# Kernel tuning notes

Hardware: AMD Instinct MI355X
Metric: run time of the kernel (lower is better)

## Reference

```python
import jax, jax.numpy as jnp
import numpy as np

HIDDEN = 2048
N_EXPERTS = 8
TOP_K = 2
MOE_INTER = 1408
NORM_TOPK = False  # config.norm_topk_prob


def setup_inputs() -> dict:
    key = jax.random.key(0)
    k0, k1, k2, k3, k4 = jax.random.split(key, 5)
    hidden_states = jax.random.normal(k0, (2, 2048, HIDDEN), dtype=jnp.float32)
    # router gate: nn.Linear(hidden, num_experts, bias=False) -> store as [H, E]
    gate_w = jax.random.normal(k1, (HIDDEN, N_EXPERTS), dtype=jnp.float32) * 0.02
    # per-expert MLP weights, stacked over experts (Linear is x @ W.T, stored pre-transposed)
    w_gate = jax.random.normal(k2, (N_EXPERTS, HIDDEN, MOE_INTER), dtype=jnp.float32) * 0.02
    w_up = jax.random.normal(k3, (N_EXPERTS, HIDDEN, MOE_INTER), dtype=jnp.float32) * 0.02
    w_down = jax.random.normal(k4, (N_EXPERTS, MOE_INTER, HIDDEN), dtype=jnp.float32) * 0.02
    return {"hidden_states": hidden_states, "gate_w": gate_w,
            "w_gate": w_gate, "w_up": w_up, "w_down": w_down}


def reference(hidden_states, gate_w, w_gate, w_up, w_down):
    B, S, H = hidden_states.shape
    x = hidden_states.reshape(-1, H)                      # [T, H]
    T = x.shape[0]
    router_logits = x @ gate_w                            # [T, E]
    probs = jax.nn.softmax(router_logits.astype(jnp.float32), axis=-1)
    routing_weights, selected = jax.lax.top_k(probs, TOP_K)  # [T, K], [T, K]
    if NORM_TOPK:
        routing_weights = routing_weights / routing_weights.sum(-1, keepdims=True)
    routing_weights = routing_weights.astype(x.dtype)
    # dense combine weights [T, E]: scatter top-k weights to expert slots
    combine = jnp.zeros((T, N_EXPERTS), dtype=x.dtype)
    combine = combine.at[jnp.arange(T)[:, None], selected].add(routing_weights)
    # run all experts densely (reference form of gather-MLP-scatter)
    g = jnp.einsum('th,ehf->tef', x, w_gate)              # [T, E, F]
    u = jnp.einsum('th,ehf->tef', x, w_up)
    h = jax.nn.silu(g) * u
    y = jnp.einsum('tef,efh->teh', h, w_down)             # [T, E, H]
    out = jnp.einsum('te,teh->th', combine, y)            # [T, H]
    return out
```

## Files before the change

kernel.cpp:

```cpp
#include <hip/hip_runtime.h>
#include <hip/hip_bf16.h>

#define HID  2048
#define NEXP 8
#define FINT 1408
#define TM   128
#define BK   32
#define GU_NPAN 88
#define DN_NPAN 64

typedef __bf16 bf16_t;
typedef __bf16 bf16x8 __attribute__((ext_vector_type(8)));
typedef float  f32x4  __attribute__((ext_vector_type(4)));

#define AS1 __attribute__((address_space(1)))
#define AS3 __attribute__((address_space(3)))

__device__ __forceinline__ void gll16(const void* g, void* l) {
    __builtin_amdgcn_global_load_lds((const AS1 void*)g, (AS3 void*)l, 16, 0, 0);
}

#define VMCNT6() asm volatile("s_waitcnt vmcnt(6)" ::: "memory")
#define VMCNT0() asm volatile("s_waitcnt vmcnt(0)" ::: "memory")
#define SB0() __builtin_amdgcn_sched_barrier(0)

__global__ __launch_bounds__(64) void router_kernel(
    const float* __restrict__ x, const float* __restrict__ gw,
    int* __restrict__ cnt, int* __restrict__ topk_id, float* __restrict__ topk_w,
    bf16_t* __restrict__ xb, int T)
{
    int t = blockIdx.x;
    if (t >= T) return;
    int lane = threadIdx.x;
    float acc[NEXP];
#pragma unroll
    for (int e = 0; e < NEXP; ++e) acc[e] = 0.f;
    const float* xr = x + (size_t)t * HID;
    bf16_t* xo = xb + (size_t)t * HID;
    for (int i0 = lane * 4; i0 < HID; i0 += 256) {
        float4 xv = *(const float4*)(xr + i0);
        bf16_t b4[4] = {(bf16_t)xv.x, (bf16_t)xv.y, (bf16_t)xv.z, (bf16_t)xv.w};
        *(uint2*)(xo + i0) = *(uint2*)b4;
        float xs[4] = {xv.x, xv.y, xv.z, xv.w};
#pragma unroll
        for (int u = 0; u < 4; ++u) {
            const float4* g4 = (const float4*)(gw + (size_t)(i0 + u) * NEXP);
            float4 a = g4[0], b = g4[1];
            acc[0] += xs[u] * a.x; acc[1] += xs[u] * a.y; acc[2] += xs[u] * a.z; acc[3] += xs[u] * a.w;
            acc[4] += xs[u] * b.x; acc[5] += xs[u] * b.y; acc[6] += xs[u] * b.z; acc[7] += xs[u] * b.w;
        }
    }
#pragma unroll
    for (int d = 1; d < 64; d <<= 1) {
#pragma unroll
        for (int e = 0; e < NEXP; ++e) acc[e] += __shfl_xor(acc[e], d, 64);
    }
    float mx = acc[0];
#pragma unroll
    for (int e = 1; e < NEXP; ++e) mx = fmaxf(mx, acc[e]);
    float p[NEXP]; float s = 0.f;
#pragma unroll
    for (int e = 0; e < NEXP; ++e) { p[e] = expf(acc[e] - mx); s += p[e]; }
    float inv = 1.f / s;
    int i1 = 0;
#pragma unroll
    for (int e = 1; e < NEXP; ++e) if (acc[e] > acc[i1]) i1 = e;
    int i2 = (i1 == 0) ? 1 : 0;
#pragma unroll
    for (int e = 0; e < NEXP; ++e) if (e != i1 && acc[e] > acc[i2]) i2 = e;
    if (lane == 0) {
        topk_id[t * 2 + 0] = i1; topk_id[t * 2 + 1] = i2;
        topk_w[t * 2 + 0] = p[i1] * inv; topk_w[t * 2 + 1] = p[i2] * inv;
        atomicAdd(&cnt[i1], 1); atomicAdd(&cnt[i2], 1);
    }
}

__global__ void offsets_kernel(const int* __restrict__ cnt, int* __restrict__ offs,
                               int* __restrict__ gbase, int* __restrict__ gcount,
                               int* __restrict__ dbase, int* __restrict__ dcount,
                               int* __restrict__ gu, int* __restrict__ dn)
{
    __shared__ int gc[8], dc[8];
    int tid = threadIdx.x;
    if (tid == 0) {
        int s = 0;
        for (int e = 0; e < NEXP; ++e) { offs[e] = s; s += cnt[e]; }
        offs[NEXP] = s;
    }
    if (tid < 8) {
        int c = 0;
        for (int p = tid; p < GU_NPAN; p += 8) { int e = p / 11; c += (cnt[e] + TM - 1) / TM; }
        gc[tid] = c;
    } else if (tid < 16) {
        int x = tid - 8, c = 0;
        for (int p = x; p < DN_NPAN; p += 8) { int e = p >> 3; c += (cnt[e] + TM - 1) / TM; }
        dc[x] = c;
    }
    __syncthreads();
    if (tid < 8) {
        int base = 0;
        for (int i = 0; i < tid; ++i) base += gc[i];
        gbase[tid] = base; gcount[tid] = gc[tid];
        int k = base;
        for (int p = tid; p < GU_NPAN; p += 8) {
            int e = p / 11, fp = p - e * 11;
            int nt = (cnt[e] + TM - 1) / TM;
            for (int t = 0; t < nt; ++t) gu[k++] = (e << 10) | (fp << 6) | t;
        }
    } else if (tid < 16) {
        int x = tid - 8;
        int base = 0;
        for (int i = 0; i < x; ++i) base += dc[i];
        dbase[x] = base; dcount[x] = dc[x];
        int k = base;
        for (int p = x; p < DN_NPAN; p += 8) {
            int e = p >> 3, hp = p & 7;
            int nt = (cnt[e] + TM - 1) / TM;
            for (int t = 0; t < nt; ++t) dn[k++] = (e << 10) | (hp << 6) | t;
        }
    }
}

__global__ void scatter_kernel(
    const int* __restrict__ topk_id, const int* __restrict__ offs, int* __restrict__ fill,
    int* __restrict__ tok, int* __restrict__ slot_of, int T)
{
    int t = blockIdx.x * blockDim.x + threadIdx.x;
    if (t >= T) return;
#pragma unroll
    for (int k = 0; k < 2; ++k) {
        int e = topk_id[t * 2 + k];
        int pos = atomicAdd(&fill[e], 1);
        int slot = offs[e] + pos;
        tok[slot] = t;
        slot_of[t * 2 + k] = slot;
    }
}

__global__ __launch_bounds__(256) void cvt3_kernel(
    const float* __restrict__ wg, const float* __restrict__ wu, const float* __restrict__ wd,
    bf16_t* __restrict__ wgb, bf16_t* __restrict__ wub, bf16_t* __restrict__ wdb)
{
    const int per = NEXP * (HID / 64) * (FINT / 64);
    int b = blockIdx.x;
    const float* in; bf16_t* outb; int R, C;
    if (b < per)            { in = wg; outb = wgb; R = HID;  C = FINT; }
    else if (b < 2 * per)   { b -= per; in = wu; outb = wub; R = HID;  C = FINT; }
    else                    { b -= 2 * per; in = wd; outb = wdb; R = FINT; C = HID; }

    int tilesC = C >> 6;
    int perE = (R >> 6) * tilesC;
    int e = b / perE;
    int rem = b - e * perE;
    int tr = rem / tilesC, tc = rem - tr * tilesC;
    const float* src = in + (size_t)e * R * C + (size_t)(tr * 64) * C + tc * 64;
    bf16_t* dst = outb + (size_t)e * R * C + (size_t)(tc * 64) * R + tr * 64;

    __shared__ float tile[64][65];
    int tid = threadIdx.x;
    int rr = tid >> 4;
    int cc = (tid & 15) * 4;
#pragma unroll
    for (int i = 0; i < 4; ++i) {
        float4 v = *(const float4*)(src + (size_t)(rr + i * 16) * C + cc);
        tile[rr + i * 16][cc + 0] = v.x; tile[rr + i * 16][cc + 1] = v.y;
        tile[rr + i * 16][cc + 2] = v.z; tile[rr + i * 16][cc + 3] = v.w;
    }
    __syncthreads();
    int oc = tid >> 2;
    int og = (tid & 3) * 16;
    bf16_t* dp = dst + (size_t)oc * R + og;
    bf16x8 o0, o1;
#pragma unroll
    for (int j = 0; j < 8; ++j) { o0[j] = (bf16_t)tile[og + j][oc]; o1[j] = (bf16_t)tile[og + 8 + j][oc]; }
    *(bf16x8*)dp = o0;
    *(bf16x8*)(dp + 8) = o1;
}

__global__ __launch_bounds__(256, 2) void gateup3_kernel(
    const bf16_t* __restrict__ xb, const bf16_t* __restrict__ wgb, const bf16_t* __restrict__ wub,
    const int* __restrict__ offs, const int* __restrict__ tok,
    const int* __restrict__ gbase, const int* __restrict__ gcount, const int* __restrict__ gu,
    bf16_t* __restrict__ h_buf)
{
    __shared__ bf16_t smem[36864];
    const int tid = threadIdx.x;
    const int lane = tid & 63, w = tid >> 6;
    const int lr = lane & 15, lg = lane >> 4;
    const int rl = lane >> 2;
    const int sw8 = ((lane & 3) ^ ((lane >> 3) & 3)) * 8;
    const int ksw = (lg ^ ((lr >> 1) & 3)) * 8;

    const int xcd = blockIdx.x & 7, slot = blockIdx.x >> 3;
    const int icnt = gcount[xcd], ib = gbase[xcd];

    for (int ii = slot; ii < icnt; ii += 96) {
        const int it = gu[ib + ii];
        const int e = it >> 10, fp = (it >> 6) & 15, tr = it & 63;
        const int seg0 = offs[e];
        const int rbase = tr * TM;
        const int nvalid = min(offs[e + 1] - seg0 - rbase, TM);
        const int row0 = seg0 + rbase;
        const int f0 = fp * 128;

        const bf16_t* aP[2];
#pragma unroll
        for (int i = 0; i < 2; ++i) {
            int r = w * 32 + i * 16 + rl;
            int tk = tok[row0 + min(r, nvalid - 1)];
            aP[i] = xb + (size_t)tk * HID + sw8;
        }
        const bf16_t* bP[4];
#pragma unroll
        for (int j = 0; j < 4; ++j) {
            int br = w * 64 + j * 16 + rl;
            const bf16_t* W = (br < 128) ? wgb : wub;
            bP[j] = W + ((size_t)e * FINT + f0 + (br & 127)) * HID + sw8;
        }

        f32x4 acc[8][4];
#pragma unroll
        for (int mi = 0; mi < 8; ++mi)
#pragma unroll
            for (int ni = 0; ni < 4; ++ni) acc[mi][ni] = (f32x4){0.f, 0.f, 0.f, 0.f};

        auto STAGE = [&](int b, int kt) {
            int k0 = kt * BK;
            bf16_t* A = smem + b * 4096;
            bf16_t* B = smem + 12288 + b * 8192;
            gll16(aP[0] + k0, A + (w * 2 + 0) * 512);
            gll16(aP[1] + k0, A + (w * 2 + 1) * 512);
            gll16(bP[0] + k0, B + (w * 4 + 0) * 512);
            gll16(bP[1] + k0, B + (w * 4 + 1) * 512);
            gll16(bP[2] + k0, B + (w * 4 + 2) * 512);
            gll16(bP[3] + k0, B + (w * 4 + 3) * 512);
        };
        auto COMPUTE = [&](int b) {
            const bf16_t* A = smem + b * 4096;
            const bf16_t* B = smem + 12288 + b * 8192;
            bf16x8 bfr[4];
#pragma unroll
            for (int ni = 0; ni < 4; ++ni)
                bfr[ni] = *(const bf16x8*)&B[(w * 64 + ni * 16 + lr) * BK + ksw];
#pragma unroll
            for (int mi = 0; mi < 8; ++mi) {
                bf16x8 a = *(const bf16x8*)&A[(mi * 16 + lr) * BK + ksw];
#pragma unroll
                for (int ni = 0; ni < 4; ++ni)
                    acc[mi][ni] = __builtin_amdgcn_mfma_f32_16x16x32_bf16(a, bfr[ni], acc[mi][ni], 0, 0, 0);
            }
        };

        const int NK = HID / BK;
        STAGE(0, 0); STAGE(1, 1);
        int c0 = 0, c1 = 1, c2 = 2;
        for (int kt = 0; kt < NK - 1; ++kt) {
            SB0(); VMCNT6(); __builtin_amdgcn_s_barrier(); SB0();
            if (kt + 2 < NK) STAGE(c2, kt + 2);
            SB0();
            COMPUTE(c0);
            int t = c0; c0 = c1; c1 = c2; c2 = t;
        }
        SB0(); VMCNT0(); __builtin_amdgcn_s_barrier(); SB0();
        COMPUTE(c0);
        __syncthreads();

        if (w >= 2) {
#pragma unroll
            for (int mi = 0; mi < 8; ++mi)
#pragma unroll
                for (int ni = 0; ni < 4; ++ni)
#pragma unroll
                    for (int rr = 0; rr < 4; ++rr) {
                        int row = mi * 16 + lg * 4 + rr;
                        int col = (w - 2) * 64 + ni * 16 + lr;
                        smem[row * 128 + col] = (bf16_t)acc[mi][ni][rr];
                    }
        }
        __syncthreads();
        if (w < 2) {
#pragma unroll
            for (int mi = 0; mi < 8; ++mi)
#pragma unroll
                for (int ni = 0; ni < 4; ++ni)
#pragma unroll
                    for (int rr = 0; rr < 4; ++rr) {
                        int row = mi * 16 + lg * 4 + rr;
                        int col = w * 64 + ni * 16 + lr;
                        float g = acc[mi][ni][rr];
                        float u = (float)smem[row * 128 + col];
                        float h = (g / (1.f + __expf(-g))) * u;
                        if (row < nvalid)
                            h_buf[(size_t)(row0 + row) * FINT + f0 + col] = (bf16_t)h;
                    }
        }
        __syncthreads();
    }
}

__global__ __launch_bounds__(256, 2) void down3_kernel(
    const bf16_t* __restrict__ h_buf, const bf16_t* __restrict__ wdb,
    const int* __restrict__ offs,
    const int* __restrict__ dbase, const int* __restrict__ dcount, const int* __restrict__ dn,
    bf16_t* __restrict__ y_buf)
{
    __shared__ bf16_t smem[36864];
    const int tid = threadIdx.x;
    const int lane = tid & 63, w = tid >> 6;
    const int lr = lane & 15, lg = lane >> 4;
    const int rl = lane >> 2;
    const int sw8 = ((lane & 3) ^ ((lane >> 3) & 3)) * 8;
    const int ksw = (lg ^ ((lr >> 1) & 3)) * 8;

    const int xcd = blockIdx.x & 7, slot = blockIdx.x >> 3;
    const int icnt = dcount[xcd], ib = dbase[xcd];

    for (int ii = slot; ii < icnt; ii += 96) {
        const int it = dn[ib + ii];
        const int e = it >> 10, hp = (it >> 6) & 15, tr = it & 63;
        const int seg0 = offs[e];
        const int rbase = tr * TM;
        const int nvalid = min(offs[e + 1] - seg0 - rbase, TM);
        const int row0 = seg0 + rbase;
        const int h0 = hp * 256;

        const bf16_t* aP[2];
#pragma unroll
        for (int i = 0; i < 2; ++i) {
            int r = w * 32 + i * 16 + rl;
            aP[i] = h_buf + (size_t)(row0 + min(r, nvalid - 1)) * FINT + sw8;
        }
        const bf16_t* bP[4];
#pragma unroll
        for (int j = 0; j < 4; ++j) {
            int br = w * 64 + j * 16 + rl;
            bP[j] = wdb + ((size_t)e * HID + h0 + br) * FINT + sw8;
        }

        f32x4 acc[8][4];
#pragma unroll
        for (int mi = 0; mi < 8; ++mi)
#pragma unroll
            for (int ni = 0; ni < 4; ++ni) acc[mi][ni] = (f32x4){0.f, 0.f, 0.f, 0.f};

        auto STAGE = [&](int b, int kt) {
            int k0 = kt * BK;
            bf16_t* A = smem + b * 4096;
            bf16_t* B = smem + 12288 + b * 8192;
            gll16(aP[0] + k0, A + (w * 2 + 0) * 512);
            gll16(aP[1] + k0, A + (w * 2 + 1) * 512);
            gll16(bP[0] + k0, B + (w * 4 + 0) * 512);
            gll16(bP[1] + k0, B + (w * 4 + 1) * 512);
            gll16(bP[2] + k0, B + (w * 4 + 2) * 512);
            gll16(bP[3] + k0, B + (w * 4 + 3) * 512);
        };
        auto COMPUTE = [&](int b) {
            const bf16_t* A = smem + b * 4096;
            const bf16_t* B = smem + 12288 + b * 8192;
            bf16x8 bfr[4];
#pragma unroll
            for (int ni = 0; ni < 4; ++ni)
                bfr[ni] = *(const bf16x8*)&B[(w * 64 + ni * 16 + lr) * BK + ksw];
#pragma unroll
            for (int mi = 0; mi < 8; ++mi) {
                bf16x8 a = *(const bf16x8*)&A[(mi * 16 + lr) * BK + ksw];
#pragma unroll
                for (int ni = 0; ni < 4; ++ni)
                    acc[mi][ni] = __builtin_amdgcn_mfma_f32_16x16x32_bf16(a, bfr[ni], acc[mi][ni], 0, 0, 0);
            }
        };

        const int NK = FINT / BK;
        STAGE(0, 0); STAGE(1, 1);
        int c0 = 0, c1 = 1, c2 = 2;
        for (int kt = 0; kt < NK - 1; ++kt) {
            SB0(); VMCNT6(); __builtin_amdgcn_s_barrier(); SB0();
            if (kt + 2 < NK) STAGE(c2, kt + 2);
            SB0();
            COMPUTE(c0);
            int t = c0; c0 = c1; c1 = c2; c2 = t;
        }
        SB0(); VMCNT0(); __builtin_amdgcn_s_barrier(); SB0();
        COMPUTE(c0);

#pragma unroll
        for (int mi = 0; mi < 8; ++mi)
#pragma unroll
            for (int ni = 0; ni < 4; ++ni)
#pragma unroll
                for (int rr = 0; rr < 4; ++rr) {
                    int row = mi * 16 + lg * 4 + rr;
                    int col = w * 64 + ni * 16 + lr;
                    if (row < nvalid)
                        y_buf[(size_t)(row0 + row) * HID + h0 + col] = (bf16_t)acc[mi][ni][rr];
                }
        __syncthreads();
    }
}

__global__ __launch_bounds__(256) void combine_kernel(
    const bf16_t* __restrict__ y, const int* __restrict__ slot_of,
    const float* __restrict__ topk_w, float* __restrict__ out, int T)
{
    int t = blockIdx.x;
    int tid = threadIdx.x;
    int s0 = slot_of[t * 2], s1 = slot_of[t * 2 + 1];
    float w0 = topk_w[t * 2], w1 = topk_w[t * 2 + 1];
    const bf16x8* y0 = (const bf16x8*)(y + (size_t)s0 * HID);
    const bf16x8* y1 = (const bf16x8*)(y + (size_t)s1 * HID);
    bf16x8 v0 = y0[tid], v1 = y1[tid];
    float* op = out + (size_t)t * HID + tid * 8;
#pragma unroll
    for (int j = 0; j < 8; ++j)
        op[j] = w0 * (float)v0[j] + w1 * (float)v1[j];
}

extern "C" void kernel_launch(void* const* d_in, const int* in_sizes, int n_in,
                              void* d_out, int out_size, void* d_ws, size_t ws_size,
                              hipStream_t stream)
{
    const float* x  = (const float*)d_in[0];
    const float* gw = (const float*)d_in[1];
    const float* wg = (const float*)d_in[2];
    const float* wu = (const float*)d_in[3];
    const float* wd = (const float*)d_in[4];
    float* out = (float*)d_out;
    int T = in_sizes[0] / HID;
    int S2 = 2 * T;

    char* base = (char*)d_ws;
    int* cnt     = (int*)base;
    int* fill    = cnt + 8;
    int* offs    = cnt + 16;
    int* gbase   = cnt + 32;
    int* gcount  = cnt + 40;
    int* dbase   = cnt + 48;
    int* dcount  = cnt + 56;
    int* gu      = cnt + 64;
    int* dnl     = cnt + 1088;
    int* topk_id = cnt + 1856;
    float* topk_w = (float*)(topk_id + S2);
    int* tok     = (int*)(topk_w + S2);
    int* slot_of = tok + S2 + 256;
    size_t small_end = (size_t)((char*)(slot_of + S2) - base);
    size_t cur = (small_end + 255) & ~(size_t)255;
    auto take = [&](size_t bytes) -> size_t {
        size_t o = cur; cur += bytes; cur = (cur + 255) & ~(size_t)255; return o;
    };
    size_t wbytes = (size_t)NEXP * HID * FINT * 2;
    size_t o_xb  = take((size_t)T * HID * 2);
    size_t o_wgb = take(wbytes);
    size_t o_wub = take(wbytes);
    size_t o_wdb = take(wbytes);
    size_t o_h   = take((size_t)(S2 + 256) * FINT * 2);
    size_t o_y   = take((size_t)(S2 + 256) * HID * 2);
    (void)ws_size;

    bf16_t* xb    = (bf16_t*)(base + o_xb);
    bf16_t* wgb   = (bf16_t*)(base + o_wgb);
    bf16_t* wub   = (bf16_t*)(base + o_wub);
    bf16_t* wdb   = (bf16_t*)(base + o_wdb);
    bf16_t* h_buf = (bf16_t*)(base + o_h);
    bf16_t* y_buf = (bf16_t*)(base + o_y);

    hipMemsetAsync(base, 0, 64, stream);

    router_kernel<<<T, 64, 0, stream>>>(x, gw, cnt, topk_id, topk_w, xb, T);
    offsets_kernel<<<1, 64, 0, stream>>>(cnt, offs, gbase, gcount, dbase, dcount, gu, dnl);
    scatter_kernel<<<(T + 255) / 256, 256, 0, stream>>>(topk_id, offs, fill, tok, slot_of, T);

    int gridW = 3 * NEXP * (HID / 64) * (FINT / 64);
    cvt3_kernel<<<gridW, 256, 0, stream>>>(wg, wu, wd, wgb, wub, wdb);

    gateup3_kernel<<<768, 256, 0, stream>>>(xb, wgb, wub, offs, tok, gbase, gcount, gu, h_buf);
    down3_kernel<<<768, 256, 0, stream>>>(h_buf, wdb, offs, dbase, dcount, dnl, y_buf);
    combine_kernel<<<T, 256, 0, stream>>>(y_buf, slot_of, topk_w, out, T);
}
```

Measured before the change: 462.8 us.

## Fuse router and weight conversion, retile expert GEMMs with 2x2 warp layout

Merges the router kernel and the weight fp32-to-bf16 transpose kernel into one launch, with the router now handling four tokens per block. The gate/up GEMM moves to a 2x2 warp grid that keeps separate gate and up accumulators, so SiLU*up is applied in registers and the shared-memory round trip for the up half goes away. The down GEMM is retiled to 128-wide output panels across more blocks with higher occupancy bounds. Both GEMMs drop the hand-tuned triple-buffered vmcnt pipeline in favour of plain double buffering with __syncthreads, which may expose more memory latency.

```diff
diff --git a/kernel.cpp b/kernel.cpp
--- a/kernel.cpp
+++ b/kernel.cpp
@@ -7,7 +7,7 @@
 #define TM   128
 #define BK   32
 #define GU_NPAN 88
-#define DN_NPAN 64
+#define DN_NPAN 128
 
 typedef __bf16 bf16_t;
 typedef __bf16 bf16x8 __attribute__((ext_vector_type(8)));
@@ -20,59 +20,98 @@
     __builtin_amdgcn_global_load_lds((const AS1 void*)g, (AS3 void*)l, 16, 0, 0);
 }
 
-#define VMCNT6() asm volatile("s_waitcnt vmcnt(6)" ::: "memory")
-#define VMCNT0() asm volatile("s_waitcnt vmcnt(0)" ::: "memory")
-#define SB0() __builtin_amdgcn_sched_barrier(0)
-
-__global__ __launch_bounds__(64) void router_kernel(
+__global__ __launch_bounds__(256) void prep_kernel(
     const float* __restrict__ x, const float* __restrict__ gw,
     int* __restrict__ cnt, int* __restrict__ topk_id, float* __restrict__ topk_w,
-    bf16_t* __restrict__ xb, int T)
-{
-    int t = blockIdx.x;
-    if (t >= T) return;
-    int lane = threadIdx.x;
-    float acc[NEXP];
-#pragma unroll
-    for (int e = 0; e < NEXP; ++e) acc[e] = 0.f;
-    const float* xr = x + (size_t)t * HID;
-    bf16_t* xo = xb + (size_t)t * HID;
-    for (int i0 = lane * 4; i0 < HID; i0 += 256) {
-        float4 xv = *(const float4*)(xr + i0);
-        bf16_t b4[4] = {(bf16_t)xv.x, (bf16_t)xv.y, (bf16_t)xv.z, (bf16_t)xv.w};
-        *(uint2*)(xo + i0) = *(uint2*)b4;
-        float xs[4] = {xv.x, xv.y, xv.z, xv.w};
-#pragma unroll
-        for (int u = 0; u < 4; ++u) {
-            const float4* g4 = (const float4*)(gw + (size_t)(i0 + u) * NEXP);
-            float4 a = g4[0], b = g4[1];
-            acc[0] += xs[u] * a.x; acc[1] += xs[u] * a.y; acc[2] += xs[u] * a.z; acc[3] += xs[u] * a.w;
-            acc[4] += xs[u] * b.x; acc[5] += xs[u] * b.y; acc[6] += xs[u] * b.z; acc[7] += xs[u] * b.w;
-        }
-    }
-#pragma unroll
-    for (int d = 1; d < 64; d <<= 1) {
-#pragma unroll
-        for (int e = 0; e < NEXP; ++e) acc[e] += __shfl_xor(acc[e], d, 64);
-    }
-    float mx = acc[0];
-#pragma unroll
-    for (int e = 1; e < NEXP; ++e) mx = fmaxf(mx, acc[e]);
-    float p[NEXP]; float s = 0.f;
-#pragma unroll
-    for (int e = 0; e < NEXP; ++e) { p[e] = expf(acc[e] - mx); s += p[e]; }
-    float inv = 1.f / s;
-    int i1 = 0;
-#pragma unroll
-    for (int e = 1; e < NEXP; ++e) if (acc[e] > acc[i1]) i1 = e;
-    int i2 = (i1 == 0) ? 1 : 0;
-#pragma unroll
-    for (int e = 0; e < NEXP; ++e) if (e != i1 && acc[e] > acc[i2]) i2 = e;
-    if (lane == 0) {
-        topk_id[t * 2 + 0] = i1; topk_id[t * 2 + 1] = i2;
-        topk_w[t * 2 + 0] = p[i1] * inv; topk_w[t * 2 + 1] = p[i2] * inv;
-        atomicAdd(&cnt[i1], 1); atomicAdd(&cnt[i2], 1);
-    }
+    bf16_t* __restrict__ xb, int T,
+    const float* __restrict__ wg, const float* __restrict__ wu, const float* __restrict__ wd,
+    bf16_t* __restrict__ wgb, bf16_t* __restrict__ wub, bf16_t* __restrict__ wdb)
+{
+    const int RB = T / 4;
+    const int per = NEXP * (HID / 64) * (FINT / 64);
+    __shared__ float tile[64][65];
+
+    if ((int)blockIdx.x < RB) {
+        int tid = threadIdx.x;
+        int lane = tid & 63, w = tid >> 6;
+        int t = blockIdx.x * 4 + w;
+        if (t >= T) return;
+        float acc[NEXP];
+#pragma unroll
+        for (int e = 0; e < NEXP; ++e) acc[e] = 0.f;
+        const float* xr = x + (size_t)t * HID;
+        bf16_t* xo = xb + (size_t)t * HID;
+        for (int i0 = lane * 4; i0 < HID; i0 += 256) {
+            float4 xv = *(const float4*)(xr + i0);
+            bf16_t b4[4] = {(bf16_t)xv.x, (bf16_t)xv.y, (bf16_t)xv.z, (bf16_t)xv.w};
+            *(uint2*)(xo + i0) = *(uint2*)b4;
+            float xs[4] = {xv.x, xv.y, xv.z, xv.w};
+#pragma unroll
+            for (int u = 0; u < 4; ++u) {
+                const float4* g4 = (const float4*)(gw + (size_t)(i0 + u) * NEXP);
+                float4 a = g4[0], b = g4[1];
+                acc[0] += xs[u] * a.x; acc[1] += xs[u] * a.y; acc[2] += xs[u] * a.z; acc[3] += xs[u] * a.w;
+                acc[4] += xs[u] * b.x; acc[5] += xs[u] * b.y; acc[6] += xs[u] * b.z; acc[7] += xs[u] * b.w;
+            }
+        }
+#pragma unroll
+        for (int d = 1; d < 64; d <<= 1) {
+#pragma unroll
+            for (int e = 0; e < NEXP; ++e) acc[e] += __shfl_xor(acc[e], d, 64);
+        }
+        float mx = acc[0];
+#pragma unroll
+        for (int e = 1; e < NEXP; ++e) mx = fmaxf(mx, acc[e]);
+        float p[NEXP]; float s = 0.f;
+#pragma unroll
+        for (int e = 0; e < NEXP; ++e) { p[e] = expf(acc[e] - mx); s += p[e]; }
+        float inv = 1.f / s;
+        int i1 = 0;
+#pragma unroll
+        for (int e = 1; e < NEXP; ++e) if (acc[e] > acc[i1]) i1 = e;
+        int i2 = (i1 == 0) ? 1 : 0;
+#pragma unroll
+        for (int e = 0; e < NEXP; ++e) if (e != i1 && acc[e] > acc[i2]) i2 = e;
+        if (lane == 0) {
+            topk_id[t * 2 + 0] = i1; topk_id[t * 2 + 1] = i2;
+            topk_w[t * 2 + 0] = p[i1] * inv; topk_w[t * 2 + 1] = p[i2] * inv;
+            atomicAdd(&cnt[i1], 1); atomicAdd(&cnt[i2], 1);
+        }
+        return;
+    }
+
+    int b = blockIdx.x - RB;
+    const float* in; bf16_t* outb; int R, C;
+    if (b < per)            { in = wg; outb = wgb; R = HID;  C = FINT; }
+    else if (b < 2 * per)   { b -= per; in = wu; outb = wub; R = HID;  C = FINT; }
+    else                    { b -= 2 * per; in = wd; outb = wdb; R = FINT; C = HID; }
+
+    int tilesC = C >> 6;
+    int perE = (R >> 6) * tilesC;
+    int e = b / perE;
+    int rem = b - e * perE;
+    int tr = rem / tilesC, tc = rem - tr * tilesC;
+    const float* src = in + (size_t)e * R * C + (size_t)(tr * 64) * C + tc * 64;
+    bf16_t* dst = outb + (size_t)e * R * C + (size_t)(tc * 64) * R + tr * 64;
+
+    int tid = threadIdx.x;
+    int rr = tid >> 4;
+    int cc = (tid & 15) * 4;
+#pragma unroll
+    for (int i = 0; i < 4; ++i) {
+        float4 v = *(const float4*)(src + (size_t)(rr + i * 16) * C + cc);
+        tile[rr + i * 16][cc + 0] = v.x; tile[rr + i * 16][cc + 1] = v.y;
+        tile[rr + i * 16][cc + 2] = v.z; tile[rr + i * 16][cc + 3] = v.w;
+    }
+    __syncthreads();
+    int oc = tid >> 2;
+    int og = (tid & 3) * 16;
+    bf16_t* dp = dst + (size_t)oc * R + og;
+    bf16x8 o0, o1;
+#pragma unroll
+    for (int j = 0; j < 8; ++j) { o0[j] = (bf16_t)tile[og + j][oc]; o1[j] = (bf16_t)tile[og + 8 + j][oc]; }
+    *(bf16x8*)dp = o0;
+    *(bf16x8*)(dp + 8) = o1;
 }
 
 __global__ void offsets_kernel(const int* __restrict__ cnt, int* __restrict__ offs,
@@ -93,7 +132,7 @@
         gc[tid] = c;
     } else if (tid < 16) {
         int x = tid - 8, c = 0;
-        for (int p = x; p < DN_NPAN; p += 8) { int e = p >> 3; c += (cnt[e] + TM - 1) / TM; }
+        for (int p = x; p < DN_NPAN; p += 8) { int e = p >> 4; c += (cnt[e] + TM - 1) / TM; }
         dc[x] = c;
     }
     __syncthreads();
@@ -114,7 +153,7 @@
         dbase[x] = base; dcount[x] = dc[x];
         int k = base;
         for (int p = x; p < DN_NPAN; p += 8) {
-            int e = p >> 3, hp = p & 7;
+            int e = p >> 4, hp = p & 15;
             int nt = (cnt[e] + TM - 1) / TM;
             for (int t = 0; t < nt; ++t) dn[k++] = (e << 10) | (hp << 6) | t;
         }
@@ -137,55 +176,16 @@
     }
 }
 
-__global__ __launch_bounds__(256) void cvt3_kernel(
-    const float* __restrict__ wg, const float* __restrict__ wu, const float* __restrict__ wd,
-    bf16_t* __restrict__ wgb, bf16_t* __restrict__ wub, bf16_t* __restrict__ wdb)
-{
-    const int per = NEXP * (HID / 64) * (FINT / 64);
-    int b = blockIdx.x;
-    const float* in; bf16_t* outb; int R, C;
-    if (b < per)            { in = wg; outb = wgb; R = HID;  C = FINT; }
-    else if (b < 2 * per)   { b -= per; in = wu; outb = wub; R = HID;  C = FINT; }
-    else                    { b -= 2 * per; in = wd; outb = wdb; R = FINT; C = HID; }
-
-    int tilesC = C >> 6;
-    int perE = (R >> 6) * tilesC;
-    int e = b / perE;
-    int rem = b - e * perE;
-    int tr = rem / tilesC, tc = rem - tr * tilesC;
-    const float* src = in + (size_t)e * R * C + (size_t)(tr * 64) * C + tc * 64;
-    bf16_t* dst = outb + (size_t)e * R * C + (size_t)(tc * 64) * R + tr * 64;
-
-    __shared__ float tile[64][65];
-    int tid = threadIdx.x;
-    int rr = tid >> 4;
-    int cc = (tid & 15) * 4;
-#pragma unroll
-    for (int i = 0; i < 4; ++i) {
-        float4 v = *(const float4*)(src + (size_t)(rr + i * 16) * C + cc);
-        tile[rr + i * 16][cc + 0] = v.x; tile[rr + i * 16][cc + 1] = v.y;
-        tile[rr + i * 16][cc + 2] = v.z; tile[rr + i * 16][cc + 3] = v.w;
-    }
-    __syncthreads();
-    int oc = tid >> 2;
-    int og = (tid & 3) * 16;
-    bf16_t* dp = dst + (size_t)oc * R + og;
-    bf16x8 o0, o1;
-#pragma unroll
-    for (int j = 0; j < 8; ++j) { o0[j] = (bf16_t)tile[og + j][oc]; o1[j] = (bf16_t)tile[og + 8 + j][oc]; }
-    *(bf16x8*)dp = o0;
-    *(bf16x8*)(dp + 8) = o1;
-}
-
-__global__ __launch_bounds__(256, 2) void gateup3_kernel(
+__global__ __launch_bounds__(256, 3) void gateup5_kernel(
     const bf16_t* __restrict__ xb, const bf16_t* __restrict__ wgb, const bf16_t* __restrict__ wub,
     const int* __restrict__ offs, const int* __restrict__ tok,
     const int* __restrict__ gbase, const int* __restrict__ gcount, const int* __restrict__ gu,
     bf16_t* __restrict__ h_buf)
 {
-    __shared__ bf16_t smem[36864];
+    __shared__ bf16_t smem[24576];
     const int tid = threadIdx.x;
     const int lane = tid & 63, w = tid >> 6;
+    const int wm = w >> 1, wn = w & 1;
     const int lr = lane & 15, lg = lane >> 4;
     const int rl = lane >> 2;
     const int sw8 = ((lane & 3) ^ ((lane >> 3) & 3)) * 8;
@@ -204,109 +204,98 @@
         const int f0 = fp * 128;
 
         const bf16_t* aP[2];
+        const bf16_t* gP[2];
+        const bf16_t* uP[2];
 #pragma unroll
         for (int i = 0; i < 2; ++i) {
             int r = w * 32 + i * 16 + rl;
             int tk = tok[row0 + min(r, nvalid - 1)];
             aP[i] = xb + (size_t)tk * HID + sw8;
-        }
-        const bf16_t* bP[4];
-#pragma unroll
-        for (int j = 0; j < 4; ++j) {
-            int br = w * 64 + j * 16 + rl;
-            const bf16_t* W = (br < 128) ? wgb : wub;
-            bP[j] = W + ((size_t)e * FINT + f0 + (br & 127)) * HID + sw8;
-        }
-
-        f32x4 acc[8][4];
-#pragma unroll
-        for (int mi = 0; mi < 8; ++mi)
-#pragma unroll
-            for (int ni = 0; ni < 4; ++ni) acc[mi][ni] = (f32x4){0.f, 0.f, 0.f, 0.f};
+            gP[i] = wgb + ((size_t)e * FINT + f0 + r) * HID + sw8;
+            uP[i] = wub + ((size_t)e * FINT + f0 + r) * HID + sw8;
+        }
+
+        f32x4 accg[4][4], accu[4][4];
+#pragma unroll
+        for (int mi = 0; mi < 4; ++mi)
+#pragma unroll
+            for (int ni = 0; ni < 4; ++ni) { accg[mi][ni] = (f32x4){0,0,0,0}; accu[mi][ni] = (f32x4){0,0,0,0}; }
 
         auto STAGE = [&](int b, int kt) {
             int k0 = kt * BK;
-            bf16_t* A = smem + b * 4096;
-            bf16_t* B = smem + 12288 + b * 8192;
-            gll16(aP[0] + k0, A + (w * 2 + 0) * 512);
-            gll16(aP[1] + k0, A + (w * 2 + 1) * 512);
-            gll16(bP[0] + k0, B + (w * 4 + 0) * 512);
-            gll16(bP[1] + k0, B + (w * 4 + 1) * 512);
-            gll16(bP[2] + k0, B + (w * 4 + 2) * 512);
-            gll16(bP[3] + k0, B + (w * 4 + 3) * 512);
+            bf16_t* A  = smem + b * 4096;
+            bf16_t* Bg = smem + 8192 + b * 4096;
+            bf16_t* Bu = smem + 16384 + b * 4096;
+            gll16(aP[0] + k0, A  + (w * 2 + 0) * 512);
+            gll16(aP[1] + k0, A  + (w * 2 + 1) * 512);
+            gll16(gP[0] + k0, Bg + (w * 2 + 0) * 512);
+            gll16(gP[1] + k0, Bg + (w * 2 + 1) * 512);
+            gll16(uP[0] + k0, Bu + (w * 2 + 0) * 512);
+            gll16(uP[1] + k0, Bu + (w * 2 + 1) * 512);
         };
         auto COMPUTE = [&](int b) {
-            const bf16_t* A = smem + b * 4096;
-            const bf16_t* B = smem + 12288 + b * 8192;
-            bf16x8 bfr[4];
-#pragma unroll
-            for (int ni = 0; ni < 4; ++ni)
-                bfr[ni] = *(const bf16x8*)&B[(w * 64 + ni * 16 + lr) * BK + ksw];
-#pragma unroll
-            for (int mi = 0; mi < 8; ++mi) {
-                bf16x8 a = *(const bf16x8*)&A[(mi * 16 + lr) * BK + ksw];
-#pragma unroll
-                for (int ni = 0; ni < 4; ++ni)
-                    acc[mi][ni] = __builtin_amdgcn_mfma_f32_16x16x32_bf16(a, bfr[ni], acc[mi][ni], 0, 0, 0);
+            const bf16_t* A  = smem + b * 4096;
+            const bf16_t* Bg = smem + 8192 + b * 4096;
+            const bf16_t* Bu = smem + 16384 + b * 4096;
+            bf16x8 a[4], bg[4], bu[4];
+#pragma unroll
+            for (int mi = 0; mi < 4; ++mi)
+                a[mi] = *(const bf16x8*)&A[(wm * 64 + mi * 16 + lr) * BK + ksw];
+#pragma unroll
+            for (int ni = 0; ni < 4; ++ni) {
+                bg[ni] = *(const bf16x8*)&Bg[(wn * 64 + ni * 16 + lr) * BK + ksw];
+                bu[ni] = *(const bf16x8*)&Bu[(wn * 64 + ni * 16 + lr) * BK + ksw];
             }
+#pragma unroll
+            for (int mi = 0; mi < 4; ++mi)
+#pragma unroll
+                for (int ni = 0; ni < 4; ++ni) {
+                    accg[mi][ni] = __builtin_amdgcn_mfma_f32_16x16x32_bf16(a[mi], bg[ni], accg[mi][ni], 0, 0, 0);
+                    accu[mi][ni] = __builtin_amdgcn_mfma_f32_16x16x32_bf16(a[mi], bu[ni], accu[mi][ni], 0, 0, 0);
+                }
         };
 
         const int NK = HID / BK;
-        STAGE(0, 0); STAGE(1, 1);
-        int c0 = 0, c1 = 1, c2 = 2;
-        for (int kt = 0; kt < NK - 1; ++kt) {
-            SB0(); VMCNT6(); __builtin_amdgcn_s_barrier(); SB0();
-            if (kt + 2 < NK) STAGE(c2, kt + 2);
-            SB0();
-            COMPUTE(c0);
-            int t = c0; c0 = c1; c1 = c2; c2 = t;
-        }
-        SB0(); VMCNT0(); __builtin_amdgcn_s_barrier(); SB0();
-        COMPUTE(c0);
+        STAGE(0, 0);
+        int cur = 0;
+        for (int kt = 0; kt < NK; ++kt) {
+            __syncthreads();
+            if (kt + 1 < NK) STAGE(cur ^ 1, kt + 1);
+            COMPUTE(cur);
+            cur ^= 1;
+        }
+
+#pragma unroll
+        for (int mi = 0; mi < 4; ++mi) {
+            int rb = wm * 64 + mi * 16 + lg * 4;
+#pragma unroll
+            for (int ni = 0; ni < 4; ++ni) {
+                int col = f0 + wn * 64 + ni * 16 + lr;
+#pragma unroll
+                for (int rr = 0; rr < 4; ++rr) {
+                    int row = rb + rr;
+                    if (row < nvalid) {
+                        float g = accg[mi][ni][rr], u = accu[mi][ni][rr];
+                        float h = (g / (1.f + __expf(-g))) * u;
+                        h_buf[(size_t)(row0 + row) * FINT + col] = (bf16_t)h;
+                    }
+                }
+            }
+        }
         __syncthreads();
-
-        if (w >= 2) {
-#pragma unroll
-            for (int mi = 0; mi < 8; ++mi)
-#pragma unroll
-                for (int ni = 0; ni < 4; ++ni)
-#pragma unroll
-                    for (int rr = 0; rr < 4; ++rr) {
-                        int row = mi * 16 + lg * 4 + rr;
-                        int col = (w - 2) * 64 + ni * 16 + lr;
-                        smem[row * 128 + col] = (bf16_t)acc[mi][ni][rr];
-                    }
-        }
-        __syncthreads();
-        if (w < 2) {
-#pragma unroll
-            for (int mi = 0; mi < 8; ++mi)
-#pragma unroll
-                for (int ni = 0; ni < 4; ++ni)
-#pragma unroll
-                    for (int rr = 0; rr < 4; ++rr) {
-                        int row = mi * 16 + lg * 4 + rr;
-                        int col = w * 64 + ni * 16 + lr;
-                        float g = acc[mi][ni][rr];
-                        float u = (float)smem[row * 128 + col];
-                        float h = (g / (1.f + __expf(-g))) * u;
-                        if (row < nvalid)
-                            h_buf[(size_t)(row0 + row) * FINT + f0 + col] = (bf16_t)h;
-                    }
-        }
-        __syncthreads();
-    }
-}
-
-__global__ __launch_bounds__(256, 2) void down3_kernel(
+    }
+}
+
+__global__ __launch_bounds__(256, 4) void down5_kernel(
     const bf16_t* __restrict__ h_buf, const bf16_t* __restrict__ wdb,
     const int* __restrict__ offs,
     const int* __restrict__ dbase, const int* __restrict__ dcount, const int* __restrict__ dn,
     bf16_t* __restrict__ y_buf)
 {
-    __shared__ bf16_t smem[36864];
+    __shared__ bf16_t smem[16384];
     const int tid = threadIdx.x;
     const int lane = tid & 63, w = tid >> 6;
+    const int wm = w >> 1, wn = w & 1;
     const int lr = lane & 15, lg = lane >> 4;
     const int rl = lane >> 2;
     const int sw8 = ((lane & 3) ^ ((lane >> 3) & 3)) * 8;
@@ -315,85 +304,80 @@
     const int xcd = blockIdx.x & 7, slot = blockIdx.x >> 3;
     const int icnt = dcount[xcd], ib = dbase[xcd];
 
-    for (int ii = slot; ii < icnt; ii += 96) {
+    for (int ii = slot; ii < icnt; ii += 128) {
         const int it = dn[ib + ii];
         const int e = it >> 10, hp = (it >> 6) & 15, tr = it & 63;
         const int seg0 = offs[e];
         const int rbase = tr * TM;
         const int nvalid = min(offs[e + 1] - seg0 - rbase, TM);
         const int row0 = seg0 + rbase;
-        const int h0 = hp * 256;
+        const int h0 = hp * 128;
 
         const bf16_t* aP[2];
+        const bf16_t* bP[2];
 #pragma unroll
         for (int i = 0; i < 2; ++i) {
             int r = w * 32 + i * 16 + rl;
             aP[i] = h_buf + (size_t)(row0 + min(r, nvalid - 1)) * FINT + sw8;
-        }
-        const bf16_t* bP[4];
-#pragma unroll
-        for (int j = 0; j < 4; ++j) {
-            int br = w * 64 + j * 16 + rl;
-            bP[j] = wdb + ((size_t)e * HID + h0 + br) * FINT + sw8;
-        }
-
-        f32x4 acc[8][4];
-#pragma unroll
-        for (int mi = 0; mi < 8; ++mi)
-#pragma unroll
-            for (int ni = 0; ni < 4; ++ni) acc[mi][ni] = (f32x4){0.f, 0.f, 0.f, 0.f};
+            bP[i] = wdb + ((size_t)e * HID + h0 + r) * FINT + sw8;
+        }
+
+        f32x4 acc[4][4];
+#pragma unroll
+        for (int mi = 0; mi < 4; ++mi)
+#pragma unroll
+            for (int ni = 0; ni < 4; ++ni) acc[mi][ni] = (f32x4){0,0,0,0};
 
         auto STAGE = [&](int b, int kt) {
             int k0 = kt * BK;
             bf16_t* A = smem + b * 4096;
-            bf16_t* B = smem + 12288 + b * 8192;
+            bf16_t* B = smem + 8192 + b * 4096;
             gll16(aP[0] + k0, A + (w * 2 + 0) * 512);
             gll16(aP[1] + k0, A + (w * 2 + 1) * 512);
-            gll16(bP[0] + k0, B + (w * 4 + 0) * 512);
-            gll16(bP[1] + k0, B + (w * 4 + 1) * 512);
-            gll16(bP[2] + k0, B + (w * 4 + 2) * 512);
-            gll16(bP[3] + k0, B + (w * 4 + 3) * 512);
+            gll16(bP[0] + k0, B + (w * 2 + 0) * 512);
+            gll16(bP[1] + k0, B + (w * 2 + 1) * 512);
         };
         auto COMPUTE = [&](int b) {
             const bf16_t* A = smem + b * 4096;
-            const bf16_t* B = smem + 12288 + b * 8192;
-            bf16x8 bfr[4];
+            const bf16_t* B = smem + 8192 + b * 4096;
+            bf16x8 a[4], bb[4];
+#pragma unroll
+            for (int mi = 0; mi < 4; ++mi)
+                a[mi] = *(const bf16x8*)&A[(wm * 64 + mi * 16 + lr) * BK + ksw];
 #pragma unroll
             for (int ni = 0; ni < 4; ++ni)
-                bfr[ni] = *(const bf16x8*)&B[(w * 64 + ni * 16 + lr) * BK + ksw];
-#pragma unroll
-            for (int mi = 0; mi < 8; ++mi) {
-                bf16x8 a = *(const bf16x8*)&A[(mi * 16 + lr) * BK + ksw];
+                bb[ni] = *(const bf16x8*)&B[(wn * 64 + ni * 16 + lr) * BK + ksw];
+#pragma unroll
+            for (int mi = 0; mi < 4; ++mi)
 #pragma unroll
                 for (int ni = 0; ni < 4; ++ni)
-                    acc[mi][ni] = __builtin_amdgcn_mfma_f32_16x16x32_bf16(a, bfr[ni], acc[mi][ni], 0, 0, 0);
+                    acc[mi][ni] = __builtin_amdgcn_mfma_f32_16x16x32_bf16(a[mi], bb[ni], acc[mi][ni], 0, 0, 0);
+        };
+
+        const int NK = FINT / BK;
+        STAGE(0, 0);
+        int cur = 0;
+        for (int kt = 0; kt < NK; ++kt) {
+            __syncthreads();
+            if (kt + 1 < NK) STAGE(cur ^ 1, kt + 1);
+            COMPUTE(cur);
+            cur ^= 1;
+        }
+
+#pragma unroll
+        for (int mi = 0; mi < 4; ++mi) {
+            int rb = wm * 64 + mi * 16 + lg * 4;
+#pragma unroll
+            for (int ni = 0; ni < 4; ++ni) {
+                int col = h0 + wn * 64 + ni * 16 + lr;
+#pragma unroll
+                for (int rr = 0; rr < 4; ++rr) {
+                    int row = rb + rr;
+                    if (row < nvalid)
+                        y_buf[(size_t)(row0 + row) * HID + col] = (bf16_t)acc[mi][ni][rr];
+                }
             }
-        };
-
-        const int NK = FINT / BK;
-        STAGE(0, 0); STAGE(1, 1);
-        int c0 = 0, c1 = 1, c2 = 2;
-        for (int kt = 0; kt < NK - 1; ++kt) {
-            SB0(); VMCNT6(); __builtin_amdgcn_s_barrier(); SB0();
-            if (kt + 2 < NK) STAGE(c2, kt + 2);
-            SB0();
-            COMPUTE(c0);
-            int t = c0; c0 = c1; c1 = c2; c2 = t;
-        }
-        SB0(); VMCNT0(); __builtin_amdgcn_s_barrier(); SB0();
-        COMPUTE(c0);
-
-#pragma unroll
-        for (int mi = 0; mi < 8; ++mi)
-#pragma unroll
-            for (int ni = 0; ni < 4; ++ni)
-#pragma unroll
-                for (int rr = 0; rr < 4; ++rr) {
-                    int row = mi * 16 + lg * 4 + rr;
-                    int col = w * 64 + ni * 16 + lr;
-                    if (row < nvalid)
-                        y_buf[(size_t)(row0 + row) * HID + h0 + col] = (bf16_t)acc[mi][ni][rr];
-                }
+        }
         __syncthreads();
     }
 }
@@ -438,7 +422,7 @@
     int* dcount  = cnt + 56;
     int* gu      = cnt + 64;
     int* dnl     = cnt + 1088;
-    int* topk_id = cnt + 1856;
+    int* topk_id = cnt + 2368;
     float* topk_w = (float*)(topk_id + S2);
     int* tok     = (int*)(topk_w + S2);
     int* slot_of = tok + S2 + 256;
@@ -465,14 +449,14 @@
 
     hipMemsetAsync(base, 0, 64, stream);
 
-    router_kernel<<<T, 64, 0, stream>>>(x, gw, cnt, topk_id, topk_w, xb, T);
+    int RB = T / 4;
+    int gridPrep = RB + 3 * NEXP * (HID / 64) * (FINT / 64);
+    prep_kernel<<<gridPrep, 256, 0, stream>>>(x, gw, cnt, topk_id, topk_w, xb, T,
+                                              wg, wu, wd, wgb, wub, wdb);
     offsets_kernel<<<1, 64, 0, stream>>>(cnt, offs, gbase, gcount, dbase, dcount, gu, dnl);
     scatter_kernel<<<(T + 255) / 256, 256, 0, stream>>>(topk_id, offs, fill, tok, slot_of, T);
 
-    int gridW = 3 * NEXP * (HID / 64) * (FINT / 64);
-    cvt3_kernel<<<gridW, 256, 0, stream>>>(wg, wu, wd, wgb, wub, wdb);
-
-    gateup3_kernel<<<768, 256, 0, stream>>>(xb, wgb, wub, offs, tok, gbase, gcount, gu, h_buf);
-    down3_kernel<<<768, 256, 0, stream>>>(h_buf, wdb, offs, dbase, dcount, dnl, y_buf);
+    gateup5_kernel<<<768, 256, 0, stream>>>(xb, wgb, wub, offs, tok, gbase, gcount, gu, h_buf);
+    down5_kernel<<<1024, 256, 0, stream>>>(h_buf, wdb, offs, dbase, dcount, dnl, y_buf);
     combine_kernel<<<T, 256, 0, stream>>>(y_buf, slot_of, topk_w, out, T);
 }
```

Result: slower. 509.1 us (+10.0%).
